# Kernel optimization log

Hardware: AMD Instinct MI355X
Metric: run time of the kernel (lower is better)

## Reference

```python
import jax, jax.numpy as jnp
import numpy as np

M, K, N = 1024, 32, 2048   # feature dim, components, samples
N_ITERS = 1500             # projected-gradient iterations for NNLS


def setup_inputs() -> dict:
    key = jax.random.key(0)
    k1, k2 = jax.random.split(key)
    # Nonnegative data matrix X (m, n) and nonnegative dictionary theta (m, k),
    # matching torch.abs(torch.rand(m, k)) init in the module.
    X = jax.random.uniform(k1, (M, N), dtype=jnp.float32)
    theta = jax.random.uniform(k2, (M, K), dtype=jnp.float32)
    return {"X": X, "theta": theta}


def _nnls_batched(theta, X):
    """Solve beta[:, l] = argmin_{b>=0} ||theta @ b - X[:, l]||^2 for all columns.

    Same optimization problem scipy.optimize.nnls solves per column in the
    original module, here solved for all n columns simultaneously with
    projected gradient descent (convex problem -> same minimizer; projection
    yields exact zeros on the inactive set, matching NNLS support structure).
    """
    G = theta.T @ theta                      # (k, k) Gram matrix
    L = jnp.linalg.eigvalsh(G)[-1] + 1e-6    # Lipschitz constant of the gradient
    T = theta.T @ X                          # (k, n)
    B0 = jnp.zeros_like(T)

    def body(_, B):
        return jnp.maximum(B - (G @ B - T) / L, 0.0)

    return jax.lax.fori_loop(0, N_ITERS, body, B0)


def reference(X, theta):
    # Module clamps theta to be nonnegative before the factorization solve.
    theta = jnp.maximum(theta, 0.0)
    return _nnls_batched(theta, X)   # beta: (k, n)
```

## Files before the change

### kernel.cpp

```cpp
#include <hip/hip_runtime.h>
#include <math.h>

#define M_DIM 1024
#define K_DIM 32
#define N_DIM 2048
#define ACC_ITERS 550
#define POLISH_ITERS 50
#define POW_ITERS 12

#define G_OFF   0
#define T_OFF   2048

__device__ __forceinline__ float bcast_lane(float x, int lane) {
    return __int_as_float(__builtin_amdgcn_readlane(__float_as_int(x), lane));
}

__global__ void __launch_bounds__(256) kPrep(const float* __restrict__ X,
                                             const float* __restrict__ theta,
                                             float* __restrict__ G,
                                             float* __restrict__ T) {
    __shared__ float th[512][32];
    int tid = threadIdx.x;
    int bid = blockIdx.x;

    if (bid < 32) {
        int i = bid;
        int j  = tid & 31;
        int ms = tid >> 5;
        float p = 0.f;
        for (int mq = 0; mq < 128; ++mq) {
            int m = ms * 128 + mq;
            float a = fmaxf(theta[m * K_DIM + i], 0.f);
            float b = fmaxf(theta[m * K_DIM + j], 0.f);
            p = fmaf(a, b, p);
        }
        float (*red)[32] = (float (*)[32])th;
        red[ms][j] = p;
        __syncthreads();
        if (ms == 0) {
            float s = p;
            for (int q = 1; q < 8; ++q) s += red[q][j];
            G[i * 32 + j] = s;
        }
        return;
    }

    int tb = bid - 32;
    int lc = tid & 31;
    int c  = tb * 32 + lc;
    int ms = tid >> 5;
    float acc[32];
#pragma unroll
    for (int i = 0; i < 32; ++i) acc[i] = 0.f;

    for (int ph = 0; ph < 2; ++ph) {
        for (int q = 0; q < 64; ++q) {
            int e = q * 256 + tid;
            th[e >> 5][e & 31] =
                fmaxf(theta[(ph * 512 + (e >> 5)) * K_DIM + (e & 31)], 0.f);
        }
        __syncthreads();
        for (int mq = 0; mq < 64; ++mq) {
            int m = ms * 64 + mq;
            float x = X[(ph * 512 + m) * N_DIM + c];
#pragma unroll
            for (int i = 0; i < 32; ++i) acc[i] = fmaf(th[m][i], x, acc[i]);
        }
        __syncthreads();
    }

    float* rbuf = &th[0][0];
#pragma unroll
    for (int i = 0; i < 32; ++i) rbuf[ms * 1024 + i * 32 + lc] = acc[i];
    __syncthreads();
    for (int q = 0; q < 4; ++q) {
        int e = q * 256 + tid;
        float s = 0.f;
        for (int s8 = 0; s8 < 8; ++s8) s += rbuf[s8 * 1024 + e];
        T[(e >> 5) * N_DIM + tb * 32 + (e & 31)] = s;
    }
}

__global__ void __launch_bounds__(256, 2) kPGD(const float* __restrict__ G,
                                               const float* __restrict__ T,
                                               float* __restrict__ out) {
    __shared__ float Gsh[32][33];
    __shared__ float lamsh, betash;
    int tid = threadIdx.x;
#pragma unroll
    for (int q = 0; q < 4; ++q) {
        int e = q * 256 + tid;
        Gsh[e >> 5][e & 31] = G[e];
    }
    __syncthreads();

    int i  = tid & 31;
    int wv = tid >> 6;
    int col = blockIdx.x * 4 + wv;

    float g[32];
#pragma unroll
    for (int j = 0; j < 32; ++j) g[j] = Gsh[i][j];

    if (tid < 64) {
        float v = 1.f, lam = 1.f;
        for (int p = 0; p < POW_ITERS; ++p) {
            float w = 0.f;
#pragma unroll
            for (int j = 0; j < 32; ++j) w = fmaf(g[j], bcast_lane(v, j), w);
            float n2 = w * w;
#pragma unroll
            for (int m = 1; m < 32; m <<= 1) n2 += __shfl_xor(n2, m, 32);
            lam = sqrtf(n2);
            v = w / lam;
        }
        float d = Gsh[i][i];
#pragma unroll
        for (int m = 1; m < 32; m <<= 1) d += __shfl_xor(d, m, 32);
        if (tid == 0) {
            float L  = lam + 1e-6f;
            float mu = 0.25f * (d - lam) * (1.0f / 31.0f);
            mu = fmaxf(mu, 1e-3f * L);
            float sL = sqrtf(L), sm = sqrtf(mu);
            lamsh  = L;
            betash = (sL - sm) / (sL + sm);
        }
    }
    __syncthreads();

    float invL = 1.0f / lamsh;
    float beta = betash;
    float ar[32];
#pragma unroll
    for (int j = 0; j < 32; ++j)
        ar[j] = ((j == i) ? 1.0f : 0.0f) - g[j] * invL;
    float t = T[i * N_DIM + col] * invL;

    __syncthreads();
    if (tid == 0) Gsh[0][0] = 0.f;
    __syncthreads();

    float y = 0.f, bprev = 0.f;
    for (int it = 0; it < ACC_ITERS; ++it) {
        float a0 = t, a1 = 0.f, a2 = 0.f, a3 = 0.f;
#pragma unroll
        for (int j = 0; j < 32; ++j) {
            float bj = bcast_lane(y, j);
            if ((j & 3) == 0)      a0 = fmaf(ar[j], bj, a0);
            else if ((j & 3) == 1) a1 = fmaf(ar[j], bj, a1);
            else if ((j & 3) == 2) a2 = fmaf(ar[j], bj, a2);
            else                   a3 = fmaf(ar[j], bj, a3);
        }
        float w = fmaxf((a0 + a1) + (a2 + a3), 0.f);
        y = fmaf(beta, w - bprev, w);
        bprev = w;
    }
    for (int it = 0; it < POLISH_ITERS; ++it) {
        float a0 = t, a1 = 0.f, a2 = 0.f, a3 = 0.f;
#pragma unroll
        for (int j = 0; j < 32; ++j) {
            float bj = bcast_lane(y, j);
            if ((j & 3) == 0)      a0 = fmaf(ar[j], bj, a0);
            else if ((j & 3) == 1) a1 = fmaf(ar[j], bj, a1);
            else if ((j & 3) == 2) a2 = fmaf(ar[j], bj, a2);
            else                   a3 = fmaf(ar[j], bj, a3);
        }
        y = fmaxf((a0 + a1) + (a2 + a3), 0.f);
    }

    if ((tid & 32) == 0) out[i * N_DIM + col] = y;
}

extern "C" void kernel_launch(void* const* d_in, const int* in_sizes, int n_in,
                              void* d_out, int out_size, void* d_ws, size_t ws_size,
                              hipStream_t stream) {
    const float* X     = (const float*)d_in[0];
    const float* theta = (const float*)d_in[1];
    float* ws = (float*)d_ws;
    float* G  = ws + G_OFF;
    float* T  = ws + T_OFF;

    kPrep<<<96, 256, 0, stream>>>(X, theta, G, T);
    kPGD<<<512, 256, 0, stream>>>(G, T, (float*)d_out);
}
```

Measured before the change: 217.0 us.

## Split prep into Gram/clamp and split-K T kernel with atomic accumulation

Replaces the single prep kernel with three steps. A memset zeroes T. One kernel computes G and writes a clamped copy of theta. A second kernel computes T = theta^T X split over the M dimension into 8 chunks, reading theta as broadcast float4 and combining partial sums with global atomicAdd. It also removes a redundant shared-memory write and its barriers in the PGD kernel, and pins the ar registers with empty asm so they stay in VGPRs. The aim is more parallelism in the T stage, at the cost of extra launches, atomic traffic and a summation order that is not deterministic.

Result: no change. 215.4 us (-0.8%).

```diff
diff --git a/kernel.cpp b/kernel.cpp
--- a/kernel.cpp
+++ b/kernel.cpp
@@ -8,77 +8,72 @@
 #define POLISH_ITERS 50
 #define POW_ITERS 12
 
-#define G_OFF   0
-#define T_OFF   2048
+#define G_OFF    0
+#define THC_OFF  2048
+#define T_OFF    36864
 
 __device__ __forceinline__ float bcast_lane(float x, int lane) {
     return __int_as_float(__builtin_amdgcn_readlane(__float_as_int(x), lane));
 }
 
-__global__ void __launch_bounds__(256) kPrep(const float* __restrict__ X,
-                                             const float* __restrict__ theta,
-                                             float* __restrict__ G,
-                                             float* __restrict__ T) {
-    __shared__ float th[512][32];
+__global__ void __launch_bounds__(256) kA(const float* __restrict__ theta,
+                                          float* __restrict__ G,
+                                          float* __restrict__ thc) {
     int tid = threadIdx.x;
     int bid = blockIdx.x;
 
-    if (bid < 32) {
-        int i = bid;
-        int j  = tid & 31;
-        int ms = tid >> 5;
-        float p = 0.f;
-        for (int mq = 0; mq < 128; ++mq) {
-            int m = ms * 128 + mq;
-            float a = fmaxf(theta[m * K_DIM + i], 0.f);
-            float b = fmaxf(theta[m * K_DIM + j], 0.f);
-            p = fmaf(a, b, p);
-        }
-        float (*red)[32] = (float (*)[32])th;
-        red[ms][j] = p;
-        __syncthreads();
-        if (ms == 0) {
-            float s = p;
-            for (int q = 1; q < 8; ++q) s += red[q][j];
-            G[i * 32 + j] = s;
-        }
+    if (bid >= 32) {
+        int e = (bid - 32) * 256 + tid;
+        thc[e] = fmaxf(theta[e], 0.f);
         return;
     }
 
-    int tb = bid - 32;
-    int lc = tid & 31;
-    int c  = tb * 32 + lc;
+    __shared__ float red[8][32];
+    int i  = bid;
+    int j  = tid & 31;
     int ms = tid >> 5;
+    float p = 0.f;
+    for (int mq = 0; mq < 128; ++mq) {
+        int m = ms * 128 + mq;
+        float a = fmaxf(theta[m * K_DIM + i], 0.f);
+        float b = fmaxf(theta[m * K_DIM + j], 0.f);
+        p = fmaf(a, b, p);
+    }
+    red[ms][j] = p;
+    __syncthreads();
+    if (ms == 0) {
+        float s = p;
+        for (int q = 1; q < 8; ++q) s += red[q][j];
+        G[i * 32 + j] = s;
+    }
+}
+
+__global__ void __launch_bounds__(256) kT(const float* __restrict__ X,
+                                          const float* __restrict__ thc,
+                                          float* __restrict__ T) {
+    int tid = threadIdx.x;
+    int c   = blockIdx.x * 256 + tid;
+    int m0  = blockIdx.y * 128;
+
     float acc[32];
 #pragma unroll
     for (int i = 0; i < 32; ++i) acc[i] = 0.f;
 
-    for (int ph = 0; ph < 2; ++ph) {
-        for (int q = 0; q < 64; ++q) {
-            int e = q * 256 + tid;
-            th[e >> 5][e & 31] =
-                fmaxf(theta[(ph * 512 + (e >> 5)) * K_DIM + (e & 31)], 0.f);
+    for (int m = 0; m < 128; ++m) {
+        int row = m0 + m;
+        float x = X[row * N_DIM + c];
+        const float4* t4 = reinterpret_cast<const float4*>(thc + row * K_DIM);
+#pragma unroll
+        for (int q = 0; q < 8; ++q) {
+            float4 v = t4[q];
+            acc[4 * q + 0] = fmaf(v.x, x, acc[4 * q + 0]);
+            acc[4 * q + 1] = fmaf(v.y, x, acc[4 * q + 1]);
+            acc[4 * q + 2] = fmaf(v.z, x, acc[4 * q + 2]);
+            acc[4 * q + 3] = fmaf(v.w, x, acc[4 * q + 3]);
         }
-        __syncthreads();
-        for (int mq = 0; mq < 64; ++mq) {
-            int m = ms * 64 + mq;
-            float x = X[(ph * 512 + m) * N_DIM + c];
+    }
 #pragma unroll
-            for (int i = 0; i < 32; ++i) acc[i] = fmaf(th[m][i], x, acc[i]);
-        }
-        __syncthreads();
-    }
-
-    float* rbuf = &th[0][0];
-#pragma unroll
-    for (int i = 0; i < 32; ++i) rbuf[ms * 1024 + i * 32 + lc] = acc[i];
-    __syncthreads();
-    for (int q = 0; q < 4; ++q) {
-        int e = q * 256 + tid;
-        float s = 0.f;
-        for (int s8 = 0; s8 < 8; ++s8) s += rbuf[s8 * 1024 + e];
-        T[(e >> 5) * N_DIM + tb * 32 + (e & 31)] = s;
-    }
+    for (int i = 0; i < 32; ++i) atomicAdd(&T[i * N_DIM + c], acc[i]);
 }
 
 __global__ void __launch_bounds__(256, 2) kPGD(const float* __restrict__ G,
@@ -130,15 +125,14 @@
 
     float invL = 1.0f / lamsh;
     float beta = betash;
+
     float ar[32];
 #pragma unroll
-    for (int j = 0; j < 32; ++j)
+    for (int j = 0; j < 32; ++j) {
         ar[j] = ((j == i) ? 1.0f : 0.0f) - g[j] * invL;
+        asm volatile("" : "+v"(ar[j]));
+    }
     float t = T[i * N_DIM + col] * invL;
-
-    __syncthreads();
-    if (tid == 0) Gsh[0][0] = 0.f;
-    __syncthreads();
 
     float y = 0.f, bprev = 0.f;
     for (int it = 0; it < ACC_ITERS; ++it) {
@@ -176,10 +170,13 @@
                               hipStream_t stream) {
     const float* X     = (const float*)d_in[0];
     const float* theta = (const float*)d_in[1];
-    float* ws = (float*)d_ws;
-    float* G  = ws + G_OFF;
-    float* T  = ws + T_OFF;
+    float* ws  = (float*)d_ws;
+    float* G   = ws + G_OFF;
+    float* thc = ws + THC_OFF;
+    float* T   = ws + T_OFF;
 
-    kPrep<<<96, 256, 0, stream>>>(X, theta, G, T);
+    hipMemsetAsync(T, 0, (size_t)K_DIM * N_DIM * sizeof(float), stream);
+    kA<<<160, 256, 0, stream>>>(theta, G, thc);
+    kT<<<dim3(8, 8), 256, 0, stream>>>(X, thc, T);
     kPGD<<<512, 256, 0, stream>>>(G, T, (float*)d_out);
 }
```
